# Performance work log

Hardware: AMD Instinct MI355X
Metric: run time of the kernel (lower is better)

Reference implementation:

```python
import jax, jax.numpy as jnp
import numpy as np

N, E, DIN, DOUT = 10000, 640000, 128, 256
BN_EPS = 1e-5
GIN_EPS = 0.0  # GINConv default eps, train_eps=False


def setup_inputs() -> dict:
    key = jax.random.key(0)
    ks = jax.random.split(key, 10)
    x = jax.random.normal(ks[0], (N, DIN), dtype=jnp.float32)
    edge_index = jax.random.randint(ks[1], (2, E), 0, N, dtype=jnp.int64)
    s1 = 1.0 / np.sqrt(DIN)
    s2 = 1.0 / np.sqrt(DOUT)
    return {
        "x": x,
        "edge_index": edge_index,
        "W1": jax.random.uniform(ks[2], (DIN, DOUT), jnp.float32, -s1, s1),
        "b1": jax.random.uniform(ks[3], (DOUT,), jnp.float32, -s1, s1),
        "gamma1": jnp.ones((DOUT,), jnp.float32),
        "beta1": jnp.zeros((DOUT,), jnp.float32),
        "W2": jax.random.uniform(ks[4], (DOUT, DOUT), jnp.float32, -s2, s2),
        "b2": jax.random.uniform(ks[5], (DOUT,), jnp.float32, -s2, s2),
        "gamma2": jnp.ones((DOUT,), jnp.float32),
        "beta2": jnp.zeros((DOUT,), jnp.float32),
    }


def _batchnorm(h, gamma, beta):
    # training-mode BatchNorm1d: batch statistics, biased variance
    mean = jnp.mean(h, axis=0)
    var = jnp.mean(jnp.square(h - mean), axis=0)
    return gamma * (h - mean) * jax.lax.rsqrt(var + BN_EPS) + beta


def reference(x, edge_index, W1, b1, gamma1, beta1, W2, b2, gamma2, beta2):
    src, dst = edge_index[0], edge_index[1]
    # GINConv: out_i = MLP((1+eps)*x_i + sum_{j->i} x_j)
    agg = jax.ops.segment_sum(x[src], dst, num_segments=N)  # [N, DIN]
    h = (1.0 + GIN_EPS) * x + agg
    # MLP: Linear -> BN -> ReLU -> Linear
    h = h @ W1 + b1
    h = jax.nn.relu(_batchnorm(h, gamma1, beta1))
    h = h @ W2 + b2
    # outer BN + ReLU
    return jax.nn.relu(_batchnorm(h, gamma2, beta2))
```

## Files before the change

kernel.cpp:

```cpp
#include <hip/hip_runtime.h>

#define NN 10000
#define DIN 128
#define DOUT 256
#define NB 128
#define PAD 192
#define NTILES (NN / 16)
static constexpr float BN_EPS = 1e-5f;

using short8 = __attribute__((ext_vector_type(8))) short;
using f32x4  = __attribute__((ext_vector_type(4))) float;

__device__ __forceinline__ unsigned short bf16r(float f) {
    unsigned int u = __float_as_uint(f);
    u += 0x7FFFu + ((u >> 16) & 1u);
    return (unsigned short)(u >> 16);
}
__device__ __forceinline__ float bf16f(unsigned short h) {
    return __uint_as_float((unsigned int)h << 16);
}
__device__ __forceinline__ int fragidx(int k, int n) {
    return ((k >> 5) << 13) | ((n >> 4) << 9) |
           ((((k >> 3) & 3) << 4 | (n & 15)) << 3) | (k & 7);
}

__global__ __launch_bounds__(256) void khist_prep(
    const int* __restrict__ ei, ushort* __restrict__ hist_g,
    ushort* __restrict__ rank, int E,
    const float* __restrict__ x, ushort* __restrict__ xb,
    const float* __restrict__ W1, ushort* __restrict__ w1f,
    const float* __restrict__ W2, ushort* __restrict__ w2f,
    float* __restrict__ stats) {
    const int tid = threadIdx.x;
    if (blockIdx.x < NB) {
        __shared__ int hist[NN];
        for (int i = tid; i < NN; i += 256) hist[i] = 0;
        __syncthreads();
        const int chunk = (E + NB - 1) / NB;
        const int e0 = blockIdx.x * chunk;
        const int e1 = min(e0 + chunk, E);
        for (int e = e0 + tid; e < e1; e += 256) {
            rank[e] = (ushort)atomicAdd(&hist[ei[E + e]], 1);
        }
        __syncthreads();
        ushort* dst = hist_g + (size_t)blockIdx.x * NN;
        for (int i = tid; i < NN; i += 256) dst[i] = (ushort)hist[i];
    } else {
        const int pt = (blockIdx.x - NB) * 256 + tid;
        if (pt < 8192) stats[pt] = 0.f;
        for (int i = pt; i < NN * DIN / 4; i += 32768) {
            const float4 v = reinterpret_cast<const float4*>(x)[i];
            ushort4 o;
            o.x = bf16r(v.x); o.y = bf16r(v.y);
            o.z = bf16r(v.z); o.w = bf16r(v.w);
            reinterpret_cast<ushort4*>(xb)[i] = o;
        }
        {
            const int k = pt >> 8, n = pt & 255;
            w1f[fragidx(k, n)] = bf16r(W1[pt]);
        }
        for (int i = pt; i < 256 * 256; i += 32768) {
            const int k = i >> 8, n = i & 255;
            w2f[fragidx(k, n)] = bf16r(W2[i]);
        }
    }
}

__global__ __launch_bounds__(256) void kscan_a(ushort* __restrict__ hist_g,
                                               int* __restrict__ total) {
    const int node = blockIdx.x * 256 + threadIdx.x;
    if (node >= NN) return;
    int run = 0;
#pragma unroll 8
    for (int b = 0; b < NB; ++b) {
        const int v = hist_g[(size_t)b * NN + node];
        hist_g[(size_t)b * NN + node] = (ushort)run;
        run += v;
    }
    total[node] = run;
}

__global__ __launch_bounds__(256) void kfill(const int* __restrict__ ei,
                                             const ushort* __restrict__ hist_g,
                                             const ushort* __restrict__ rank,
                                             int* __restrict__ edge_src,
                                             int E) {
    const int chunk = (E + NB - 1) / NB;
    for (int e = blockIdx.x * 256 + threadIdx.x; e < E;
         e += gridDim.x * 256) {
        const int src = ei[e];
        const int dst = ei[E + e];
        const int b = e / chunk;
        const int pos = dst * PAD + (int)hist_g[(size_t)b * NN + dst]
                        + (int)rank[e];
        edge_src[pos] = src;
    }
}

__global__ __launch_bounds__(256) void gemm1_k(
    const float* __restrict__ x, const ushort* __restrict__ xb,
    const int* __restrict__ total, const int* __restrict__ edge_src,
    const ushort* __restrict__ w1f, const float* __restrict__ b1,
    ushort* __restrict__ h1f, float* __restrict__ sum1,
    float* __restrict__ sq1) {
    __shared__ short a_lds[4 * 64 * 8];
    __shared__ float work[6208];
    short* b_lds = (short*)work;
    float* hrow  = work;
    float* red_s = work + 4160;
    float* red_q = work + 5184;
    const int tid = threadIdx.x;
    const int w = tid >> 6, l = tid & 63;
    const int m = blockIdx.x;
    const int hw = tid >> 5, c4 = tid & 31;
    const ushort4* xb4 = reinterpret_cast<const ushort4*>(xb);

#pragma unroll
    for (int r = 0; r < 2; ++r) {
        const int row = r * 8 + hw;
        const int node = m * 16 + row;
        const int beg = node * PAD;
        const int end = beg + total[node];

        float4 a0 = make_float4(0.f, 0.f, 0.f, 0.f);
        float4 a1 = a0, a2 = a0, a3 = a0;
        int j = beg;
        for (; j + 7 < end; j += 8) {
            int s[8];
#pragma unroll
            for (int t = 0; t < 8; ++t) s[t] = edge_src[j + t];
            ushort4 v[8];
#pragma unroll
            for (int t = 0; t < 8; ++t) v[t] = xb4[(size_t)s[t] * 32 + c4];
#pragma unroll
            for (int t = 0; t < 8; ++t) {
                float4* a = (t & 3) == 0 ? &a0 : (t & 3) == 1 ? &a1
                          : (t & 3) == 2 ? &a2 : &a3;
                a->x += bf16f(v[t].x);
                a->y += bf16f(v[t].y);
                a->z += bf16f(v[t].z);
                a->w += bf16f(v[t].w);
            }
        }
        for (; j < end; ++j) {
            const ushort4 v = xb4[(size_t)edge_src[j] * 32 + c4];
            a0.x += bf16f(v.x); a0.y += bf16f(v.y);
            a0.z += bf16f(v.z); a0.w += bf16f(v.w);
        }
        const float4 xv =
            reinterpret_cast<const float4*>(x)[(size_t)node * 32 + c4];
        ushort4 o;
        o.x = bf16r(xv.x + a0.x + a1.x + a2.x + a3.x);
        o.y = bf16r(xv.y + a0.y + a1.y + a2.y + a3.y);
        o.z = bf16r(xv.z + a0.z + a1.z + a2.z + a3.z);
        o.w = bf16r(xv.w + a0.w + a1.w + a2.w + a3.w);
        const int c = c4 >> 3, kg = (c4 >> 1) & 3, half = c4 & 1;
        *reinterpret_cast<ushort4*>(
            (char*)a_lds + c * 1024 + ((kg << 4) + row) * 16 + half * 8) = o;
    }

    f32x4 acc[4];
#pragma unroll
    for (int p = 0; p < 4; ++p) {
        const float b = b1[(w * 4 + p) * 16 + (l & 15)];
        acc[p] = (f32x4){b, b, b, b};
    }

    for (int c = 0; c < 4; ++c) {
        __syncthreads();
        const float4* src = ((const float4*)w1f) + c * 1024;
#pragma unroll
        for (int i = 0; i < 4; ++i)
            ((float4*)b_lds)[tid + 256 * i] = src[tid + 256 * i];
        __syncthreads();
        const short8 a = ((const short8*)a_lds)[c * 64 + l];
#pragma unroll
        for (int p = 0; p < 4; ++p) {
            const short8 b = ((const short8*)b_lds)[(w * 4 + p) * 64 + l];
            acc[p] = __builtin_amdgcn_mfma_f32_16x16x32_bf16(a, b, acc[p],
                                                             0, 0, 0);
        }
    }
    __syncthreads();

#pragma unroll
    for (int p = 0; p < 4; ++p) {
        const int col = (w * 4 + p) * 16 + (l & 15);
        float s = 0.f, q = 0.f;
#pragma unroll
        for (int r = 0; r < 4; ++r) {
            const float v = acc[p][r];
            hrow[((l >> 4) * 4 + r) * 260 + col] = v;
            s += v;
            q += v * v;
        }
        red_s[(l >> 4) * 256 + col] = s;
        red_q[(l >> 4) * 256 + col] = q;
    }
    __syncthreads();
    {
        float s = 0.f, q = 0.f;
#pragma unroll
        for (int g = 0; g < 4; ++g) {
            s += red_s[g * 256 + tid];
            q += red_q[g * 256 + tid];
        }
        atomicAdd(&sum1[(m & 7) * 256 + tid], s);
        atomicAdd(&sq1[(m & 7) * 256 + tid], q);
    }
#pragma unroll
    for (int t = 0; t < 2; ++t) {
        const int u = tid + t * 256;
        const int c2 = u >> 6, kg = (u >> 4) & 3, row = u & 15;
        const float* src = &hrow[row * 260 + c2 * 32 + kg * 8];
        short8 g;
#pragma unroll
        for (int jj = 0; jj < 8; ++jj) g[jj] = (short)bf16r(src[jj]);
        ((short8*)h1f)[m * 512 + u] = g;
    }
}

__global__ __launch_bounds__(256) void gemm2_k(
    const ushort* __restrict__ h1f, const float* __restrict__ sum1,
    const float* __restrict__ sq1, const float* __restrict__ gamma1,
    const float* __restrict__ beta1, const ushort* __restrict__ w2f,
    const float* __restrict__ b2, float* __restrict__ h2,
    float* __restrict__ sum2, float* __restrict__ sq2) {
    __shared__ short a_lds[8 * 64 * 8];
    __shared__ float work[6208];
    __shared__ float sc1[DOUT], sh1[DOUT];
    short* b_lds = (short*)work;
    float* hrow  = work;
    float* red_s = work + 4160;
    float* red_q = work + 5184;
    const int tid = threadIdx.x;
    const int w = tid >> 6, l = tid & 63;
    const int m = blockIdx.x;

    {
        float s = 0.f, q = 0.f;
#pragma unroll
        for (int i = 0; i < 8; ++i) {
            s += sum1[i * 256 + tid];
            q += sq1[i * 256 + tid];
        }
        const float nInv = 1.0f / (float)NN;
        const float mean = s * nInv;
        const float var = q * nInv - mean * mean;
        const float sc = gamma1[tid] * rsqrtf(var + BN_EPS);
        sc1[tid] = sc;
        sh1[tid] = beta1[tid] - mean * sc;
    }
    __syncthreads();

#pragma unroll
    for (int t = 0; t < 2; ++t) {
        const int u = tid + 256 * t;
        const int col0 = ((u >> 6) << 5) + (((u >> 4) & 3) << 3);
        const short8 hv = ((const short8*)h1f)[m * 512 + u];
        short8 g;
#pragma unroll
        for (int jj = 0; jj < 8; ++jj) {
            const float f = bf16f((unsigned short)hv[jj]);
            const float r = fmaxf(fmaf(f, sc1[col0 + jj], sh1[col0 + jj]), 0.f);
            g[jj] = (short)bf16r(r);
        }
        ((short8*)a_lds)[u] = g;
    }

    f32x4 acc[4];
#pragma unroll
    for (int p = 0; p < 4; ++p) {
        const float b = b2[(w * 4 + p) * 16 + (l & 15)];
        acc[p] = (f32x4){b, b, b, b};
    }

    for (int c = 0; c < 8; ++c) {
        __syncthreads();
        const float4* src = ((const float4*)w2f) + c * 1024;
#pragma unroll
        for (int i = 0; i < 4; ++i)
            ((float4*)b_lds)[tid + 256 * i] = src[tid + 256 * i];
        __syncthreads();
        const short8 a = ((const short8*)a_lds)[c * 64 + l];
#pragma unroll
        for (int p = 0; p < 4; ++p) {
            const short8 b = ((const short8*)b_lds)[(w * 4 + p) * 64 + l];
            acc[p] = __builtin_amdgcn_mfma_f32_16x16x32_bf16(a, b, acc[p],
                                                             0, 0, 0);
        }
    }
    __syncthreads();

#pragma unroll
    for (int p = 0; p < 4; ++p) {
        const int col = (w * 4 + p) * 16 + (l & 15);
        float s = 0.f, q = 0.f;
#pragma unroll
        for (int r = 0; r < 4; ++r) {
            const float v = acc[p][r];
            hrow[((l >> 4) * 4 + r) * 260 + col] = v;
            s += v;
            q += v * v;
        }
        red_s[(l >> 4) * 256 + col] = s;
        red_q[(l >> 4) * 256 + col] = q;
    }
    __syncthreads();
    {
        float s = 0.f, q = 0.f;
#pragma unroll
        for (int g = 0; g < 4; ++g) {
            s += red_s[g * 256 + tid];
            q += red_q[g * 256 + tid];
        }
        atomicAdd(&sum2[(m & 7) * 256 + tid], s);
        atomicAdd(&sq2[(m & 7) * 256 + tid], q);
    }
#pragma unroll
    for (int i = 0; i < 4; ++i) {
        const int idx = tid + 256 * i;
        const int row = idx >> 6, col4 = idx & 63;
        const float4 v = *(const float4*)&hrow[row * 260 + col4 * 4];
        ((float4*)h2)[(size_t)(m * 16 + row) * 64 + col4] = v;
    }
}

__global__ __launch_bounds__(256) void bn_relu_out_k(
    const float* __restrict__ h2, const float* __restrict__ sum2,
    const float* __restrict__ sq2, const float* __restrict__ gamma2,
    const float* __restrict__ beta2, float* __restrict__ out) {
    __shared__ float sc2[DOUT], sh2[DOUT];
    const int tid = threadIdx.x;
    {
        float s = 0.f, q = 0.f;
#pragma unroll
        for (int i = 0; i < 8; ++i) {
            s += sum2[i * 256 + tid];
            q += sq2[i * 256 + tid];
        }
        const float nInv = 1.0f / (float)NN;
        const float mean = s * nInv;
        const float var = q * nInv - mean * mean;
        const float sc = gamma2[tid] * rsqrtf(var + BN_EPS);
        sc2[tid] = sc;
        sh2[tid] = beta2[tid] - mean * sc;
    }
    __syncthreads();
#pragma unroll
    for (int i = 0; i < 4; ++i) {
        const int u = blockIdx.x * 1024 + i * 256 + tid;
        const int k4 = u & 63;
        const float4 h = reinterpret_cast<const float4*>(h2)[u];
        const float4 sc = reinterpret_cast<const float4*>(sc2)[k4];
        const float4 sh = reinterpret_cast<const float4*>(sh2)[k4];
        float4 g;
        g.x = fmaxf(fmaf(h.x, sc.x, sh.x), 0.f);
        g.y = fmaxf(fmaf(h.y, sc.y, sh.y), 0.f);
        g.z = fmaxf(fmaf(h.z, sc.z, sh.z), 0.f);
        g.w = fmaxf(fmaf(h.w, sc.w, sh.w), 0.f);
        reinterpret_cast<float4*>(out)[u] = g;
    }
}

extern "C" void kernel_launch(void* const* d_in, const int* in_sizes, int n_in,
                              void* d_out, int out_size, void* d_ws,
                              size_t ws_size, hipStream_t stream) {
    const float* x      = (const float*)d_in[0];
    const int*   ei     = (const int*)d_in[1];
    const float* W1     = (const float*)d_in[2];
    const float* b1     = (const float*)d_in[3];
    const float* gamma1 = (const float*)d_in[4];
    const float* beta1  = (const float*)d_in[5];
    const float* W2     = (const float*)d_in[6];
    const float* b2     = (const float*)d_in[7];
    const float* gamma2 = (const float*)d_in[8];
    const float* beta2  = (const float*)d_in[9];
    const int E = in_sizes[1] / 2;

    char* w = (char*)d_ws;
    size_t off = 0;
    float* stats = (float*)(w + off); off += 32768;
    float* sum1 = stats + 0;
    float* sq1  = stats + 2048;
    float* sum2 = stats + 4096;
    float* sq2  = stats + 6144;
    ushort* hist_g = (ushort*)(w + off); off += (size_t)NB * NN * 2;
    ushort* rank   = (ushort*)(w + off); off += (size_t)E * 2;
    int* total    = (int*)(w + off); off += 40064;
    int* edge_src = (int*)(w + off); off += (size_t)NN * PAD * 4;
    ushort* xb    = (ushort*)(w + off); off += (size_t)NN * DIN * 2;
    ushort* w1f   = (ushort*)(w + off); off += 65536;
    ushort* w2f   = (ushort*)(w + off); off += 131072;
    ushort* h1f   = (ushort*)(w + off); off += (size_t)NN * DOUT * 2;
    float* h2     = (float*)(w + off); off += (size_t)NN * DOUT * 4;
    float* out    = (float*)d_out;

    khist_prep<<<2 * NB, 256, 0, stream>>>(ei, hist_g, rank, E, x, xb,
                                           W1, w1f, W2, w2f, stats);
    kscan_a<<<40, 256, 0, stream>>>(hist_g, total);
    kfill<<<256, 256, 0, stream>>>(ei, hist_g, rank, edge_src, E);
    gemm1_k<<<NTILES, 256, 0, stream>>>(x, xb, total, edge_src, w1f, b1,
                                        h1f, sum1, sq1);
    gemm2_k<<<NTILES, 256, 0, stream>>>(h1f, sum1, sq1, gamma1, beta1, w2f,
                                        b2, h2, sum2, sq2);
    bn_relu_out_k<<<NN * DOUT / 4 / 1024, 256, 0, stream>>>(h2, sum2, sq2,
                                                            gamma2, beta2, out);
}
```

Before: 79.35 us.

## Store h2 as bf16, interleave two-node gathers, halve histogram blocks

The pre-BN intermediate h2 is now stored as bf16, which halves its write traffic in gemm2 and its read traffic in the final BN/ReLU kernel. Normalisation still uses statistics accumulated in fp32 before rounding. The gather in gemm1 now walks the neighbour lists of both nodes of each half-warp at once, so more independent loads are in flight per thread. The histogram block count drops from 128 to 64, which shortens the per-node scan at the cost of more work per histogram block. Rounding h2 to bf16 adds some extra error to the output.

Measured after the change: 78.71 us. No clear change (-0.8%).

```diff
diff --git a/kernel.cpp b/kernel.cpp
--- a/kernel.cpp
+++ b/kernel.cpp
@@ -3,7 +3,8 @@
 #define NN 10000
 #define DIN 128
 #define DOUT 256
-#define NB 128
+#define NB 64
+#define NPREP 128
 #define PAD 192
 #define NTILES (NN / 16)
 static constexpr float BN_EPS = 1e-5f;
@@ -48,7 +49,7 @@
     } else {
         const int pt = (blockIdx.x - NB) * 256 + tid;
         if (pt < 8192) stats[pt] = 0.f;
-        for (int i = pt; i < NN * DIN / 4; i += 32768) {
+        for (int i = pt; i < NN * DIN / 4; i += NPREP * 256) {
             const float4 v = reinterpret_cast<const float4*>(x)[i];
             ushort4 o;
             o.x = bf16r(v.x); o.y = bf16r(v.y);
@@ -59,7 +60,7 @@
             const int k = pt >> 8, n = pt & 255;
             w1f[fragidx(k, n)] = bf16r(W1[pt]);
         }
-        for (int i = pt; i < 256 * 256; i += 32768) {
+        for (int i = pt; i < 256 * 256; i += NPREP * 256) {
             const int k = i >> 8, n = i & 255;
             w2f[fragidx(k, n)] = bf16r(W2[i]);
         }
@@ -115,48 +116,98 @@
     const int hw = tid >> 5, c4 = tid & 31;
     const ushort4* xb4 = reinterpret_cast<const ushort4*>(xb);
 
-#pragma unroll
-    for (int r = 0; r < 2; ++r) {
-        const int row = r * 8 + hw;
-        const int node = m * 16 + row;
-        const int beg = node * PAD;
-        const int end = beg + total[node];
-
-        float4 a0 = make_float4(0.f, 0.f, 0.f, 0.f);
-        float4 a1 = a0, a2 = a0, a3 = a0;
-        int j = beg;
-        for (; j + 7 < end; j += 8) {
-            int s[8];
-#pragma unroll
-            for (int t = 0; t < 8; ++t) s[t] = edge_src[j + t];
-            ushort4 v[8];
-#pragma unroll
-            for (int t = 0; t < 8; ++t) v[t] = xb4[(size_t)s[t] * 32 + c4];
-#pragma unroll
-            for (int t = 0; t < 8; ++t) {
-                float4* a = (t & 3) == 0 ? &a0 : (t & 3) == 1 ? &a1
-                          : (t & 3) == 2 ? &a2 : &a3;
-                a->x += bf16f(v[t].x);
-                a->y += bf16f(v[t].y);
-                a->z += bf16f(v[t].z);
-                a->w += bf16f(v[t].w);
-            }
-        }
-        for (; j < end; ++j) {
-            const ushort4 v = xb4[(size_t)edge_src[j] * 32 + c4];
-            a0.x += bf16f(v.x); a0.y += bf16f(v.y);
-            a0.z += bf16f(v.z); a0.w += bf16f(v.w);
-        }
+    const int nodeA = m * 16 + hw;
+    const int nodeB = nodeA + 8;
+    const int begA = nodeA * PAD, endA = begA + total[nodeA];
+    const int begB = nodeB * PAD, endB = begB + total[nodeB];
+
+    float4 aA[4], aB[4];
+#pragma unroll
+    for (int t = 0; t < 4; ++t) {
+        aA[t] = make_float4(0.f, 0.f, 0.f, 0.f);
+        aB[t] = aA[t];
+    }
+    int jA = begA, jB = begB;
+    for (; jA + 3 < endA && jB + 3 < endB; jA += 4, jB += 4) {
+        int sA[4], sB[4];
+#pragma unroll
+        for (int t = 0; t < 4; ++t) {
+            sA[t] = edge_src[jA + t];
+            sB[t] = edge_src[jB + t];
+        }
+        ushort4 vA[4], vB[4];
+#pragma unroll
+        for (int t = 0; t < 4; ++t) {
+            vA[t] = xb4[(size_t)sA[t] * 32 + c4];
+            vB[t] = xb4[(size_t)sB[t] * 32 + c4];
+        }
+#pragma unroll
+        for (int t = 0; t < 4; ++t) {
+            aA[t].x += bf16f(vA[t].x); aA[t].y += bf16f(vA[t].y);
+            aA[t].z += bf16f(vA[t].z); aA[t].w += bf16f(vA[t].w);
+            aB[t].x += bf16f(vB[t].x); aB[t].y += bf16f(vB[t].y);
+            aB[t].z += bf16f(vB[t].z); aB[t].w += bf16f(vB[t].w);
+        }
+    }
+    for (; jA + 3 < endA; jA += 4) {
+        int s[4];
+#pragma unroll
+        for (int t = 0; t < 4; ++t) s[t] = edge_src[jA + t];
+        ushort4 v[4];
+#pragma unroll
+        for (int t = 0; t < 4; ++t) v[t] = xb4[(size_t)s[t] * 32 + c4];
+#pragma unroll
+        for (int t = 0; t < 4; ++t) {
+            aA[t].x += bf16f(v[t].x); aA[t].y += bf16f(v[t].y);
+            aA[t].z += bf16f(v[t].z); aA[t].w += bf16f(v[t].w);
+        }
+    }
+    for (; jA < endA; ++jA) {
+        const ushort4 v = xb4[(size_t)edge_src[jA] * 32 + c4];
+        aA[0].x += bf16f(v.x); aA[0].y += bf16f(v.y);
+        aA[0].z += bf16f(v.z); aA[0].w += bf16f(v.w);
+    }
+    for (; jB + 3 < endB; jB += 4) {
+        int s[4];
+#pragma unroll
+        for (int t = 0; t < 4; ++t) s[t] = edge_src[jB + t];
+        ushort4 v[4];
+#pragma unroll
+        for (int t = 0; t < 4; ++t) v[t] = xb4[(size_t)s[t] * 32 + c4];
+#pragma unroll
+        for (int t = 0; t < 4; ++t) {
+            aB[t].x += bf16f(v[t].x); aB[t].y += bf16f(v[t].y);
+            aB[t].z += bf16f(v[t].z); aB[t].w += bf16f(v[t].w);
+        }
+    }
+    for (; jB < endB; ++jB) {
+        const ushort4 v = xb4[(size_t)edge_src[jB] * 32 + c4];
+        aB[0].x += bf16f(v.x); aB[0].y += bf16f(v.y);
+        aB[0].z += bf16f(v.z); aB[0].w += bf16f(v.w);
+    }
+
+    const int c = c4 >> 3, kg = (c4 >> 1) & 3, half = c4 & 1;
+    {
         const float4 xv =
-            reinterpret_cast<const float4*>(x)[(size_t)node * 32 + c4];
+            reinterpret_cast<const float4*>(x)[(size_t)nodeA * 32 + c4];
         ushort4 o;
-        o.x = bf16r(xv.x + a0.x + a1.x + a2.x + a3.x);
-        o.y = bf16r(xv.y + a0.y + a1.y + a2.y + a3.y);
-        o.z = bf16r(xv.z + a0.z + a1.z + a2.z + a3.z);
-        o.w = bf16r(xv.w + a0.w + a1.w + a2.w + a3.w);
-        const int c = c4 >> 3, kg = (c4 >> 1) & 3, half = c4 & 1;
+        o.x = bf16r(xv.x + aA[0].x + aA[1].x + aA[2].x + aA[3].x);
+        o.y = bf16r(xv.y + aA[0].y + aA[1].y + aA[2].y + aA[3].y);
+        o.z = bf16r(xv.z + aA[0].z + aA[1].z + aA[2].z + aA[3].z);
+        o.w = bf16r(xv.w + aA[0].w + aA[1].w + aA[2].w + aA[3].w);
         *reinterpret_cast<ushort4*>(
-            (char*)a_lds + c * 1024 + ((kg << 4) + row) * 16 + half * 8) = o;
+            (char*)a_lds + c * 1024 + ((kg << 4) + hw) * 16 + half * 8) = o;
+    }
+    {
+        const float4 xv =
+            reinterpret_cast<const float4*>(x)[(size_t)nodeB * 32 + c4];
+        ushort4 o;
+        o.x = bf16r(xv.x + aB[0].x + aB[1].x + aB[2].x + aB[3].x);
+        o.y = bf16r(xv.y + aB[0].y + aB[1].y + aB[2].y + aB[3].y);
+        o.z = bf16r(xv.z + aB[0].z + aB[1].z + aB[2].z + aB[3].z);
+        o.w = bf16r(xv.w + aB[0].w + aB[1].w + aB[2].w + aB[3].w);
+        *reinterpret_cast<ushort4*>(
+            (char*)a_lds + c * 1024 + ((kg << 4) + 8 + hw) * 16 + half * 8) = o;
     }
 
     f32x4 acc[4];
@@ -166,14 +217,14 @@
         acc[p] = (f32x4){b, b, b, b};
     }
 
-    for (int c = 0; c < 4; ++c) {
-        __syncthreads();
-        const float4* src = ((const float4*)w1f) + c * 1024;
+    for (int cc = 0; cc < 4; ++cc) {
+        __syncthreads();
+        const float4* src = ((const float4*)w1f) + cc * 1024;
 #pragma unroll
         for (int i = 0; i < 4; ++i)
             ((float4*)b_lds)[tid + 256 * i] = src[tid + 256 * i];
         __syncthreads();
-        const short8 a = ((const short8*)a_lds)[c * 64 + l];
+        const short8 a = ((const short8*)a_lds)[cc * 64 + l];
 #pragma unroll
         for (int p = 0; p < 4; ++p) {
             const short8 b = ((const short8*)b_lds)[(w * 4 + p) * 64 + l];
@@ -211,8 +262,8 @@
 #pragma unroll
     for (int t = 0; t < 2; ++t) {
         const int u = tid + t * 256;
-        const int c2 = u >> 6, kg = (u >> 4) & 3, row = u & 15;
-        const float* src = &hrow[row * 260 + c2 * 32 + kg * 8];
+        const int c2 = u >> 6, kg2 = (u >> 4) & 3, row = u & 15;
+        const float* src = &hrow[row * 260 + c2 * 32 + kg2 * 8];
         short8 g;
 #pragma unroll
         for (int jj = 0; jj < 8; ++jj) g[jj] = (short)bf16r(src[jj]);
@@ -224,7 +275,7 @@
     const ushort* __restrict__ h1f, const float* __restrict__ sum1,
     const float* __restrict__ sq1, const float* __restrict__ gamma1,
     const float* __restrict__ beta1, const ushort* __restrict__ w2f,
-    const float* __restrict__ b2, float* __restrict__ h2,
+    const float* __restrict__ b2, ushort* __restrict__ h2b,
     float* __restrict__ sum2, float* __restrict__ sq2) {
     __shared__ short a_lds[8 * 64 * 8];
     __shared__ float work[6208];
@@ -318,16 +369,24 @@
         atomicAdd(&sq2[(m & 7) * 256 + tid], q);
     }
 #pragma unroll
-    for (int i = 0; i < 4; ++i) {
+    for (int i = 0; i < 2; ++i) {
         const int idx = tid + 256 * i;
-        const int row = idx >> 6, col4 = idx & 63;
-        const float4 v = *(const float4*)&hrow[row * 260 + col4 * 4];
-        ((float4*)h2)[(size_t)(m * 16 + row) * 64 + col4] = v;
+        const int row = idx >> 5, col8 = idx & 31;
+        const float* src = &hrow[row * 260 + col8 * 8];
+        ushort4 lo, hi;
+        lo.x = bf16r(src[0]); lo.y = bf16r(src[1]);
+        lo.z = bf16r(src[2]); lo.w = bf16r(src[3]);
+        hi.x = bf16r(src[4]); hi.y = bf16r(src[5]);
+        hi.z = bf16r(src[6]); hi.w = bf16r(src[7]);
+        reinterpret_cast<ushort4*>(h2b)[((size_t)(m * 16 + row) * 64 +
+                                         col8 * 2)] = lo;
+        reinterpret_cast<ushort4*>(h2b)[((size_t)(m * 16 + row) * 64 +
+                                         col8 * 2 + 1)] = hi;
     }
 }
 
 __global__ __launch_bounds__(256) void bn_relu_out_k(
-    const float* __restrict__ h2, const float* __restrict__ sum2,
+    const ushort* __restrict__ h2b, const float* __restrict__ sum2,
     const float* __restrict__ sq2, const float* __restrict__ gamma2,
     const float* __restrict__ beta2, float* __restrict__ out) {
     __shared__ float sc2[DOUT], sh2[DOUT];
@@ -351,14 +410,14 @@
     for (int i = 0; i < 4; ++i) {
         const int u = blockIdx.x * 1024 + i * 256 + tid;
         const int k4 = u & 63;
-        const float4 h = reinterpret_cast<const float4*>(h2)[u];
+        const ushort4 hv = reinterpret_cast<const ushort4*>(h2b)[u];
         const float4 sc = reinterpret_cast<const float4*>(sc2)[k4];
         const float4 sh = reinterpret_cast<const float4*>(sh2)[k4];
         float4 g;
-        g.x = fmaxf(fmaf(h.x, sc.x, sh.x), 0.f);
-        g.y = fmaxf(fmaf(h.y, sc.y, sh.y), 0.f);
-        g.z = fmaxf(fmaf(h.z, sc.z, sh.z), 0.f);
-        g.w = fmaxf(fmaf(h.w, sc.w, sh.w), 0.f);
+        g.x = fmaxf(fmaf(bf16f(hv.x), sc.x, sh.x), 0.f);
+        g.y = fmaxf(fmaf(bf16f(hv.y), sc.y, sh.y), 0.f);
+        g.z = fmaxf(fmaf(bf16f(hv.z), sc.z, sh.z), 0.f);
+        g.w = fmaxf(fmaf(bf16f(hv.w), sc.w, sh.w), 0.f);
         reinterpret_cast<float4*>(out)[u] = g;
     }
 }
@@ -393,17 +452,17 @@
     ushort* w1f   = (ushort*)(w + off); off += 65536;
     ushort* w2f   = (ushort*)(w + off); off += 131072;
     ushort* h1f   = (ushort*)(w + off); off += (size_t)NN * DOUT * 2;
-    float* h2     = (float*)(w + off); off += (size_t)NN * DOUT * 4;
+    ushort* h2b   = (ushort*)(w + off); off += (size_t)NN * DOUT * 2;
     float* out    = (float*)d_out;
 
-    khist_prep<<<2 * NB, 256, 0, stream>>>(ei, hist_g, rank, E, x, xb,
-                                           W1, w1f, W2, w2f, stats);
+    khist_prep<<<NB + NPREP, 256, 0, stream>>>(ei, hist_g, rank, E, x, xb,
+                                               W1, w1f, W2, w2f, stats);
     kscan_a<<<40, 256, 0, stream>>>(hist_g, total);
     kfill<<<256, 256, 0, stream>>>(ei, hist_g, rank, edge_src, E);
     gemm1_k<<<NTILES, 256, 0, stream>>>(x, xb, total, edge_src, w1f, b1,
                                         h1f, sum1, sq1);
     gemm2_k<<<NTILES, 256, 0, stream>>>(h1f, sum1, sq1, gamma1, beta1, w2f,
-                                        b2, h2, sum2, sq2);
-    bn_relu_out_k<<<NN * DOUT / 4 / 1024, 256, 0, stream>>>(h2, sum2, sq2,
+                                        b2, h2b, sum2, sq2);
+    bn_relu_out_k<<<NN * DOUT / 4 / 1024, 256, 0, stream>>>(h2b, sum2, sq2,
                                                             gamma2, beta2, out);
 }
```
